# Kernel tuning notes

Measured on AMD Instinct MI355X. Metric: run time of the kernel, lower is better.

## Reference

```python
import jax, jax.numpy as jnp
import numpy as np

B, N, M, C_IN, C_OUT = 8, 1024, 1024, 8, 16
C_REP = C_IN + 1  # density channel + in_channels


def setup_inputs() -> dict:
    key = jax.random.key(0)
    ks = jax.random.split(key, 6)
    x = jax.random.normal(ks[0], (B, N, 1), dtype=jnp.float32)
    y = jax.random.normal(ks[1], (B, N, C_IN), dtype=jnp.float32)
    t = jax.random.normal(ks[2], (B, M, 1), dtype=jnp.float32)
    # sigma initialised as log(init_length_scale) * ones(in_channels+1)
    sigma = jnp.full((C_REP,), np.log(0.1), dtype=jnp.float32)
    W = jax.random.normal(ks[3], (C_OUT, C_REP), dtype=jnp.float32) / np.sqrt(C_REP)
    b = jnp.zeros((C_OUT,), dtype=jnp.float32)
    return {"x": x, "y": y, "t": t, "sigma": sigma, "W": W, "b": b}


def reference(x, y, t, sigma, W, b):
    # pairwise squared distances: (B, N, M)
    dists = (x - jnp.swapaxes(t, 1, 2)) ** 2
    # RBF weights with per-channel length scales: (B, N, M, C_REP)
    scales = jnp.exp(sigma)  # (C_REP,)
    wt = jnp.exp(-0.5 * dists[..., None] / scales**2)
    # prepend density channel of ones to y: (B, N, C_REP)
    y_rep = jnp.concatenate([jnp.ones_like(y[..., :1]), y], axis=-1)
    # weighted sum over context points n -> (B, M, C_REP)
    y_out = jnp.sum(y_rep[:, :, None, :] * wt, axis=1)
    density, conv = y_out[..., :1], y_out[..., 1:]
    y_out = jnp.concatenate([density, conv / (density + 1e-8)], axis=-1)
    # pointwise linear: (B, M, C_OUT)
    return jnp.einsum("bmc,oc->bmo", y_out, W) + b
```

## Files before the change

kernel.cpp:

```cpp
#include <hip/hip_runtime.h>


#define B_    8
#define N_    1024
#define M_    1024
#define CIN   8
#define COUT  16
#define CREP  9
#define MTILE 16
#define NGRP  16
#define KITER (N_ / NGRP)

#if __has_builtin(__builtin_amdgcn_exp2f)
#define EXP2F(v) __builtin_amdgcn_exp2f(v)
#else
#define EXP2F(v) exp2f(v)
#endif

__global__ __launch_bounds__(256) void convcnp_kernel(
    const float* __restrict__ x,
    const float* __restrict__ y,
    const float* __restrict__ t,
    const float* __restrict__ sigma,
    const float* __restrict__ W,
    const float* __restrict__ bias,
    float* __restrict__ out)
{
    __shared__ float x_lds[N_];
    __shared__ float y_lds[N_ * CIN];
    __shared__ float red[4][MTILE][CREP];
    __shared__ float fin[MTILE][CREP];

    const int tid  = threadIdx.x;
    const int bb   = blockIdx.x >> 6;
    const int tile = blockIdx.x & 63;
    const int m0   = tile * MTILE;

    const float4* x4  = (const float4*)(x + bb * N_);
    float4*       xl4 = (float4*)x_lds;
    xl4[tid] = x4[tid];
    const float4* y4  = (const float4*)(y + bb * N_ * CIN);
    float4*       yl4 = (float4*)y_lds;
#pragma unroll
    for (int j = 0; j < 8; ++j) yl4[tid + j * 256] = y4[tid + j * 256];

    float kc[CREP];
#pragma unroll
    for (int c = 0; c < CREP; ++c)
        kc[c] = -0.72134752044f * EXP2F(-2.88539008178f * sigma[c]);
    bool uni = true;
#pragma unroll
    for (int c = 1; c < CREP; ++c) uni = uni && (kc[c] == kc[0]);

    const int   m_loc = tid & 15;
    const int   g     = tid >> 4;
    const float tv    = t[bb * M_ + m0 + m_loc];

    float acc[CREP];
#pragma unroll
    for (int c = 0; c < CREP; ++c) acc[c] = 0.f;

    __syncthreads();

    if (uni) {
        const float k0 = kc[0];
#pragma unroll 4
        for (int k = 0; k < KITER; ++k) {
            const int    n  = g + (k << 4);
            const float  xv = x_lds[n];
            const float4 ya = *(const float4*)(y_lds + n * CIN);
            const float4 yb = *(const float4*)(y_lds + n * CIN + 4);
            float d = xv - tv; d *= d;
            const float w = EXP2F(k0 * d);
            acc[0] += w;
            acc[1] += ya.x * w; acc[2] += ya.y * w;
            acc[3] += ya.z * w; acc[4] += ya.w * w;
            acc[5] += yb.x * w; acc[6] += yb.y * w;
            acc[7] += yb.z * w; acc[8] += yb.w * w;
        }
    } else {
#pragma unroll 2
        for (int k = 0; k < KITER; ++k) {
            const int    n  = g + (k << 4);
            const float  xv = x_lds[n];
            const float4 ya = *(const float4*)(y_lds + n * CIN);
            const float4 yb = *(const float4*)(y_lds + n * CIN + 4);
            float d = xv - tv; d *= d;
            const float yr[CREP] = {1.f, ya.x, ya.y, ya.z, ya.w,
                                         yb.x, yb.y, yb.z, yb.w};
#pragma unroll
            for (int c = 0; c < CREP; ++c)
                acc[c] += yr[c] * EXP2F(kc[c] * d);
        }
    }

#pragma unroll
    for (int c = 0; c < CREP; ++c) {
        acc[c] += __shfl_xor(acc[c], 16, 64);
        acc[c] += __shfl_xor(acc[c], 32, 64);
    }
    const int w_id = tid >> 6;
    const int lane = tid & 63;
    if (lane < MTILE) {
#pragma unroll
        for (int c = 0; c < CREP; ++c) red[w_id][lane][c] = acc[c];
    }
    __syncthreads();

    for (int idx = tid; idx < MTILE * CREP; idx += 256) {
        const int m = idx / CREP, c = idx - m * CREP;
        fin[m][c] = red[0][m][c] + red[1][m][c] + red[2][m][c] + red[3][m][c];
    }
    __syncthreads();

    const int o = tid & 15;
    const int m = tid >> 4;
    const float dens = fin[m][0];
    const float inv  = 1.0f / (dens + 1e-8f);
    float r = bias[o] + W[o * CREP] * dens;
#pragma unroll
    for (int c = 1; c < CREP; ++c) r += W[o * CREP + c] * (fin[m][c] * inv);
    out[(bb * M_ + m0 + m) * COUT + o] = r;
}

extern "C" void kernel_launch(void* const* d_in, const int* in_sizes, int n_in,
                              void* d_out, int out_size, void* d_ws, size_t ws_size,
                              hipStream_t stream) {
    const float* x     = (const float*)d_in[0];
    const float* y     = (const float*)d_in[1];
    const float* t     = (const float*)d_in[2];
    const float* sigma = (const float*)d_in[3];
    const float* W     = (const float*)d_in[4];
    const float* bias  = (const float*)d_in[5];
    float*       out   = (float*)d_out;

    convcnp_kernel<<<dim3(B_ * (M_ / MTILE)), dim3(256), 0, stream>>>(
        x, y, t, sigma, W, bias, out);
}
```

Measured before the change: 70.17 us.

## Split context dimension across blocks and register-block two targets per thread

The N reduction is split into two halves handled by separate blocks, which write partial sums to workspace. A second kernel adds the halves and applies normalization and the linear projection. Each thread now handles two target points so every loaded x/y sample is reused twice, and blocks stage only half of the context into LDS. The cost is an extra kernel launch, a global round trip for the partials, and more registers per thread.

New measurement: 71.35 us. No clear change (+1.7%).

```diff
diff --git a/kernel.cpp b/kernel.cpp
--- a/kernel.cpp
+++ b/kernel.cpp
@@ -1,15 +1,19 @@
 #include <hip/hip_runtime.h>
 
 
-#define B_    8
-#define N_    1024
-#define M_    1024
-#define CIN   8
-#define COUT  16
-#define CREP  9
-#define MTILE 16
-#define NGRP  16
-#define KITER (N_ / NGRP)
+#define B_     8
+#define N_     1024
+#define M_     1024
+#define CIN    8
+#define COUT   16
+#define CREP   9
+#define NSPLIT 2
+#define NCHUNK (N_ / NSPLIT)
+#define LM     8
+#define GN     32
+#define RM     2
+#define MTILE  (LM * RM)
+#define KITER  (NCHUNK / GN)
 
 #if __has_builtin(__builtin_amdgcn_exp2f)
 #define EXP2F(v) __builtin_amdgcn_exp2f(v)
@@ -17,32 +21,32 @@
 #define EXP2F(v) exp2f(v)
 #endif
 
-__global__ __launch_bounds__(256) void convcnp_kernel(
+__global__ __launch_bounds__(256) void convcnp_partial(
     const float* __restrict__ x,
     const float* __restrict__ y,
     const float* __restrict__ t,
     const float* __restrict__ sigma,
-    const float* __restrict__ W,
-    const float* __restrict__ bias,
-    float* __restrict__ out)
+    float* __restrict__ P)
 {
-    __shared__ float x_lds[N_];
-    __shared__ float y_lds[N_ * CIN];
-    __shared__ float red[4][MTILE][CREP];
-    __shared__ float fin[MTILE][CREP];
+    __shared__ float x_lds[NCHUNK];
+    __shared__ float y_lds[NCHUNK * CIN];
+    __shared__ float red[4][LM][RM][CREP];
 
     const int tid  = threadIdx.x;
-    const int bb   = blockIdx.x >> 6;
     const int tile = blockIdx.x & 63;
+    const int s    = (blockIdx.x >> 6) & (NSPLIT - 1);
+    const int bb   = blockIdx.x >> 7;
     const int m0   = tile * MTILE;
+    const int n0   = s * NCHUNK;
 
-    const float4* x4  = (const float4*)(x + bb * N_);
+    const float4* x4  = (const float4*)(x + bb * N_ + n0);
     float4*       xl4 = (float4*)x_lds;
-    xl4[tid] = x4[tid];
-    const float4* y4  = (const float4*)(y + bb * N_ * CIN);
+    if (tid < NCHUNK / 4) xl4[tid] = x4[tid];
+    const float4* y4  = (const float4*)(y + (bb * N_ + n0) * CIN);
     float4*       yl4 = (float4*)y_lds;
 #pragma unroll
-    for (int j = 0; j < 8; ++j) yl4[tid + j * 256] = y4[tid + j * 256];
+    for (int j = 0; j < NCHUNK * CIN / 4 / 256; ++j)
+        yl4[tid + j * 256] = y4[tid + j * 256];
 
     float kc[CREP];
 #pragma unroll
@@ -52,13 +56,16 @@
 #pragma unroll
     for (int c = 1; c < CREP; ++c) uni = uni && (kc[c] == kc[0]);
 
-    const int   m_loc = tid & 15;
-    const int   g     = tid >> 4;
-    const float tv    = t[bb * M_ + m0 + m_loc];
+    const int   ml = tid & (LM - 1);
+    const int   g  = tid >> 3;
+    const float t0 = t[bb * M_ + m0 + ml];
+    const float t1 = t[bb * M_ + m0 + ml + LM];
 
-    float acc[CREP];
+    float acc[RM][CREP];
 #pragma unroll
-    for (int c = 0; c < CREP; ++c) acc[c] = 0.f;
+    for (int r = 0; r < RM; ++r)
+#pragma unroll
+        for (int c = 0; c < CREP; ++c) acc[r][c] = 0.f;
 
     __syncthreads();
 
@@ -66,61 +73,88 @@
         const float k0 = kc[0];
 #pragma unroll 4
         for (int k = 0; k < KITER; ++k) {
-            const int    n  = g + (k << 4);
+            const int    n  = g + (k << 5);
             const float  xv = x_lds[n];
             const float4 ya = *(const float4*)(y_lds + n * CIN);
             const float4 yb = *(const float4*)(y_lds + n * CIN + 4);
-            float d = xv - tv; d *= d;
-            const float w = EXP2F(k0 * d);
-            acc[0] += w;
-            acc[1] += ya.x * w; acc[2] += ya.y * w;
-            acc[3] += ya.z * w; acc[4] += ya.w * w;
-            acc[5] += yb.x * w; acc[6] += yb.y * w;
-            acc[7] += yb.z * w; acc[8] += yb.w * w;
+            float d0 = xv - t0; d0 *= d0;
+            float d1 = xv - t1; d1 *= d1;
+            const float w0 = EXP2F(k0 * d0);
+            const float w1 = EXP2F(k0 * d1);
+            acc[0][0] += w0;
+            acc[0][1] += ya.x * w0; acc[0][2] += ya.y * w0;
+            acc[0][3] += ya.z * w0; acc[0][4] += ya.w * w0;
+            acc[0][5] += yb.x * w0; acc[0][6] += yb.y * w0;
+            acc[0][7] += yb.z * w0; acc[0][8] += yb.w * w0;
+            acc[1][0] += w1;
+            acc[1][1] += ya.x * w1; acc[1][2] += ya.y * w1;
+            acc[1][3] += ya.z * w1; acc[1][4] += ya.w * w1;
+            acc[1][5] += yb.x * w1; acc[1][6] += yb.y * w1;
+            acc[1][7] += yb.z * w1; acc[1][8] += yb.w * w1;
         }
     } else {
 #pragma unroll 2
         for (int k = 0; k < KITER; ++k) {
-            const int    n  = g + (k << 4);
+            const int    n  = g + (k << 5);
             const float  xv = x_lds[n];
             const float4 ya = *(const float4*)(y_lds + n * CIN);
             const float4 yb = *(const float4*)(y_lds + n * CIN + 4);
-            float d = xv - tv; d *= d;
+            float d0 = xv - t0; d0 *= d0;
+            float d1 = xv - t1; d1 *= d1;
             const float yr[CREP] = {1.f, ya.x, ya.y, ya.z, ya.w,
                                          yb.x, yb.y, yb.z, yb.w};
 #pragma unroll
-            for (int c = 0; c < CREP; ++c)
-                acc[c] += yr[c] * EXP2F(kc[c] * d);
+            for (int c = 0; c < CREP; ++c) {
+                acc[0][c] += yr[c] * EXP2F(kc[c] * d0);
+                acc[1][c] += yr[c] * EXP2F(kc[c] * d1);
+            }
         }
     }
 
+    const int wave = tid >> 6;
+    const int lane = tid & 63;
 #pragma unroll
-    for (int c = 0; c < CREP; ++c) {
-        acc[c] += __shfl_xor(acc[c], 16, 64);
-        acc[c] += __shfl_xor(acc[c], 32, 64);
-    }
-    const int w_id = tid >> 6;
-    const int lane = tid & 63;
-    if (lane < MTILE) {
+    for (int r = 0; r < RM; ++r)
 #pragma unroll
-        for (int c = 0; c < CREP; ++c) red[w_id][lane][c] = acc[c];
-    }
+        for (int c = 0; c < CREP; ++c) {
+            float v = acc[r][c];
+            v += __shfl_xor(v, 8, 64);
+            v += __shfl_xor(v, 16, 64);
+            v += __shfl_xor(v, 32, 64);
+            if (lane < LM) red[wave][lane][r][c] = v;
+        }
     __syncthreads();
 
-    for (int idx = tid; idx < MTILE * CREP; idx += 256) {
-        const int m = idx / CREP, c = idx - m * CREP;
-        fin[m][c] = red[0][m][c] + red[1][m][c] + red[2][m][c] + red[3][m][c];
+    if (tid < MTILE * CREP) {
+        const int mm = tid / CREP;
+        const int c  = tid - mm * CREP;
+        const int r  = mm >> 3, l = mm & 7;
+        const float v = red[0][l][r][c] + red[1][l][r][c] +
+                        red[2][l][r][c] + red[3][l][r][c];
+        P[((s * B_ + bb) * M_ + m0 + mm) * CREP + c] = v;
     }
-    __syncthreads();
+}
 
-    const int o = tid & 15;
-    const int m = tid >> 4;
-    const float dens = fin[m][0];
+__global__ __launch_bounds__(256) void convcnp_proj(
+    const float* __restrict__ P,
+    const float* __restrict__ W,
+    const float* __restrict__ bias,
+    float* __restrict__ out)
+{
+    const int gid = blockIdx.x * 256 + threadIdx.x;
+    const int o   = gid & (COUT - 1);
+    const int bm  = gid >> 4;
+    const float* p0 = P + bm * CREP;
+    const float* p1 = P + (size_t)B_ * M_ * CREP + bm * CREP;
+    float p[CREP];
+#pragma unroll
+    for (int c = 0; c < CREP; ++c) p[c] = p0[c] + p1[c];
+    const float dens = p[0];
     const float inv  = 1.0f / (dens + 1e-8f);
     float r = bias[o] + W[o * CREP] * dens;
 #pragma unroll
-    for (int c = 1; c < CREP; ++c) r += W[o * CREP + c] * (fin[m][c] * inv);
-    out[(bb * M_ + m0 + m) * COUT + o] = r;
+    for (int c = 1; c < CREP; ++c) r += W[o * CREP + c] * (p[c] * inv);
+    out[gid] = r;
 }
 
 extern "C" void kernel_launch(void* const* d_in, const int* in_sizes, int n_in,
@@ -133,7 +167,10 @@
     const float* W     = (const float*)d_in[4];
     const float* bias  = (const float*)d_in[5];
     float*       out   = (float*)d_out;
+    float*       P     = (float*)d_ws;
 
-    convcnp_kernel<<<dim3(B_ * (M_ / MTILE)), dim3(256), 0, stream>>>(
-        x, y, t, sigma, W, bias, out);
+    convcnp_partial<<<dim3(B_ * (M_ / MTILE) * NSPLIT), dim3(256), 0, stream>>>(
+        x, y, t, sigma, P);
+    convcnp_proj<<<dim3(B_ * M_ * COUT / 256), dim3(256), 0, stream>>>(
+        P, W, bias, out);
 }
```
